# Optimization experiments

Measured on AMD Instinct MI355X. Metric: run time of the kernel, lower is better.

## Reference

```python
import jax, jax.numpy as jnp
import numpy as np

N_HEADS = 4
HEAD_DIM = 128
FMAP_H, FMAP_W = 32, 32
IN_DIM = 512
BATCH = 16


def setup_inputs() -> dict:
    key = jax.random.key(0)
    k1, k2, k3, k4 = jax.random.split(key, 4)
    scale = HEAD_DIM ** (-0.5)
    x = jax.random.normal(k1, (BATCH, IN_DIM, FMAP_H, FMAP_W), dtype=jnp.float32)
    # 1x1 conv weight producing q,k,v stacked along output channels
    conv_w = jax.random.normal(k2, (3 * N_HEADS * HEAD_DIM, IN_DIM), dtype=jnp.float32) * (IN_DIM ** -0.5)
    pos_h = jax.random.normal(k3, (FMAP_H, HEAD_DIM), dtype=jnp.float32) * scale
    pos_w = jax.random.normal(k4, (FMAP_W, HEAD_DIM), dtype=jnp.float32) * scale
    return {"x": x, "conv_w": conv_w, "pos_h": pos_h, "pos_w": pos_w}


def reference(x, conv_w, pos_h, pos_w):
    B, C, H, W = x.shape
    hw = H * W
    scale = HEAD_DIM ** (-0.5)
    # 1x1 conv == pointwise linear over channels
    qkv = jnp.einsum('bchw,oc->bohw', x, conv_w)               # [B, 3*nh*hd, H, W]
    qkv = qkv.reshape(B, 3, N_HEADS, HEAD_DIM, hw)             # chunk + per-head split
    q = jnp.swapaxes(qkv[:, 0], -1, -2) * scale                # [B, nh, hw, hd]
    k = jnp.swapaxes(qkv[:, 1], -1, -2)
    v = jnp.swapaxes(qkv[:, 2], -1, -2)
    # absolute positional embedding: h[i,:]+w[j,:] flattened over positions
    emb = (pos_h[:, None, :] + pos_w[None, :, :]).reshape(hw, HEAD_DIM)
    sim = jnp.einsum('bhid,bhjd->bhij', q, k) + jnp.einsum('bhid,jd->bhij', q, emb)
    attn = jax.nn.softmax(sim, axis=-1)
    out = jnp.einsum('bhij,bhjd->bhid', attn, v)               # [B, nh, hw, hd]
    out = jnp.swapaxes(out, -1, -2)                            # [B, nh, hd, hw]
    return out.reshape(B, N_HEADS * HEAD_DIM, hw // N_HEADS, N_HEADS)
```

## Files before the change

kernel.cpp:

```cpp
#include <hip/hip_runtime.h>

#define NB 16
#define NH 4
#define HD 128
#define HW 1024
#define CIN 512

typedef short s16x8 __attribute__((ext_vector_type(8)));
typedef short s16x4 __attribute__((ext_vector_type(4)));
typedef float f32x4 __attribute__((ext_vector_type(4)));

static __device__ __forceinline__ short f2bf(float f) {
    union { float f; unsigned u; } v; v.f = f;
    unsigned r = v.u + 0x7fffu + ((v.u >> 16) & 1u);
    return (short)(r >> 16);
}

static __device__ __forceinline__ void gload16(const short* g, short* l) {
    __builtin_amdgcn_global_load_lds(
        (const __attribute__((address_space(1))) unsigned int*)g,
        (__attribute__((address_space(3))) unsigned int*)l, 16, 0, 0);
}

__global__ __launch_bounds__(256) void prep_xw(
    const float* __restrict__ x, const float* __restrict__ w,
    short* __restrict__ xT, short* __restrict__ Wb)
{
    int blk = blockIdx.x;
    if (blk < NB * 16 * 32) {
        int b = blk >> 9, rem = blk & 511;
        int ct = rem >> 5, pt = rem & 31;
        __shared__ float tile[32][33];
        int tc = threadIdx.x >> 5;
        int tp = threadIdx.x & 31;
        const float* xb = x + ((size_t)b * CIN + ct * 32) * HW + pt * 32;
        #pragma unroll
        for (int i = 0; i < 4; i++)
            tile[tc + i * 8][tp] = xb[(size_t)(tc + i * 8) * HW + tp];
        __syncthreads();
        int p = threadIdx.x >> 3, cq = threadIdx.x & 7;
        short* xo = xT + ((size_t)b * HW + pt * 32 + p) * CIN + ct * 32 + cq * 4;
        s16x4 o4 = { f2bf(tile[cq * 4 + 0][p]), f2bf(tile[cq * 4 + 1][p]),
                     f2bf(tile[cq * 4 + 2][p]), f2bf(tile[cq * 4 + 3][p]) };
        *reinterpret_cast<s16x4*>(xo) = o4;
    } else {
        int wb = blk - NB * 16 * 32;
        size_t base = (size_t)wb * 1024 + threadIdx.x * 4;
        const float4 v = *reinterpret_cast<const float4*>(w + base);
        s16x4 o4 = { f2bf(v.x), f2bf(v.y), f2bf(v.z), f2bf(v.w) };
        *reinterpret_cast<s16x4*>(Wb + base) = o4;
    }
}

__global__ __launch_bounds__(256, 2) void qkv_proj(
    const short* __restrict__ xT, const short* __restrict__ Wb,
    const float* __restrict__ pos_h, const float* __restrict__ pos_w,
    short* __restrict__ Q, short* __restrict__ Kp, short* __restrict__ Vt)
{
    __shared__ __align__(1024) char smem[65536];
    short* As = (short*)smem;
    short* Bs = As + 2 * 128 * 64;
    short* vb = (short*)smem;
    short* T  = (short*)smem;

    const int pt = blockIdx.x, ot = blockIdx.y, b = blockIdx.z;
    const int tid = threadIdx.x;
    const int wave = tid >> 6, lane = tid & 63;
    const int l16 = lane & 15, quad = lane >> 4;
    const int wm = (wave & 1) * 64, wn = (wave >> 1) * 64;
    const int o0 = ot * 128, p0 = pt * 128;

    const short* xb = xT + (size_t)b * HW * CIN;

    const int r8 = lane >> 3, c8 = lane & 7;
    const int sch = c8 ^ r8;
    const short* wsrc = Wb + (size_t)(o0 + wave * 32 + r8) * CIN + sch * 8;
    const short* xsrc = xb + (size_t)(p0 + wave * 32 + r8) * CIN + sch * 8;

    f32x4 acc[4][4];
    #pragma unroll
    for (int i = 0; i < 4; i++)
        #pragma unroll
        for (int j = 0; j < 4; j++)
            acc[i][j] = f32x4{0.f, 0.f, 0.f, 0.f};

    #define STAGE_AB(buf, step)                                               \
        do {                                                                  \
            int kc_ = (step) * 64;                                            \
            short* ad_ = As + (buf) * 8192 + wave * 2048;                     \
            short* bd_ = Bs + (buf) * 8192 + wave * 2048;                     \
            _Pragma("unroll")                                                 \
            for (int j = 0; j < 4; j++) {                                     \
                gload16(wsrc + kc_ + (size_t)(j * 8) * CIN, ad_ + j * 512);   \
                gload16(xsrc + kc_ + (size_t)(j * 8) * CIN, bd_ + j * 512);   \
            }                                                                 \
        } while (0)

    STAGE_AB(0, 0);
    __syncthreads();

    #pragma unroll 1
    for (int st = 0; st < 8; st++) {
        const int cur = st & 1, nxt = cur ^ 1;
        const short* as = As + cur * 8192;
        const short* bs = Bs + cur * 8192;

        STAGE_AB(nxt, (st + 1) & 7);

        #pragma unroll
        for (int kk = 0; kk < 2; kk++) {
            s16x8 aF[4], bF[4];
            #pragma unroll
            for (int mi = 0; mi < 4; mi++)
                aF[mi] = *(const s16x8*)(as + (wm + mi * 16 + l16) * 64
                                         + (((kk * 4 + quad) ^ (l16 & 7)) * 8));
            #pragma unroll
            for (int ni = 0; ni < 4; ni++)
                bF[ni] = *(const s16x8*)(bs + (wn + ni * 16 + l16) * 64
                                         + (((kk * 4 + quad) ^ (l16 & 7)) * 8));
            #pragma unroll
            for (int mi = 0; mi < 4; mi++)
                #pragma unroll
                for (int ni = 0; ni < 4; ni++)
                    acc[mi][ni] = __builtin_amdgcn_mfma_f32_16x16x32_bf16(
                        aF[mi], bF[ni], acc[mi][ni], 0, 0, 0);
        }
        __syncthreads();
    }
    #undef STAGE_AB

    const int s = ot >> 2, h = ot & 3;
    const size_t bh = (size_t)(b * NH + h);

    if (s < 2) {
        const float qs = 0.08838834764831845f * 1.4426950408889634f;
        #pragma unroll
        for (int mi = 0; mi < 4; mi++) {
            int col = wm + mi * 16 + quad * 4;
            int chunk = col >> 3, sub = (quad & 1) * 4;
            #pragma unroll
            for (int ni = 0; ni < 4; ni++) {
                int row = wn + ni * 16 + l16;
                f32x4 a = acc[mi][ni];
                s16x4 o4;
                if (s == 0) {
                    o4 = s16x4{ f2bf(a.x * qs), f2bf(a.y * qs),
                                f2bf(a.z * qs), f2bf(a.w * qs) };
                } else {
                    int p = p0 + row;
                    const float4 eh = *reinterpret_cast<const float4*>(pos_h + (p >> 5) * HD + col);
                    const float4 ew = *reinterpret_cast<const float4*>(pos_w + (p & 31) * HD + col);
                    o4 = s16x4{ f2bf(a.x + eh.x + ew.x), f2bf(a.y + eh.y + ew.y),
                                f2bf(a.z + eh.z + ew.z), f2bf(a.w + eh.w + ew.w) };
                }
                *(s16x4*)(T + row * 128 + ((chunk ^ (l16 & 7)) * 8 + sub)) = o4;
            }
        }
        __syncthreads();
        short* Ob = (s == 0 ? Q : Kp) + bh * (size_t)(HW * HD) + (size_t)p0 * HD;
        #pragma unroll
        for (int j = 0; j < 8; j++) {
            int row = j * 16 + (tid >> 4);
            int c16 = tid & 15;
            s16x8 v8 = *(const s16x8*)(T + row * 128 + ((c16 ^ ((tid >> 4) & 7)) * 8));
            *reinterpret_cast<s16x8*>(Ob + (size_t)row * HD + c16 * 8) = v8;
        }
    } else {
        __syncthreads();
        #pragma unroll
        for (int mi = 0; mi < 4; mi++) {
            int d0 = wm + mi * 16 + quad * 4;
            #pragma unroll
            for (int ni = 0; ni < 4; ni++) {
                int p = wn + ni * 16 + l16;
                f32x4 a = acc[mi][ni];
                int g = p >> 5, u = p & 31;
                int slot = g * 32 + ((u & 15) >> 2) * 8 + (u >> 4) * 4 + 0;
                (void)slot;
                vb[(d0 + 0) * 136 + p] = f2bf(a.x);
                vb[(d0 + 1) * 136 + p] = f2bf(a.y);
                vb[(d0 + 2) * 136 + p] = f2bf(a.z);
                vb[(d0 + 3) * 136 + p] = f2bf(a.w);
            }
        }
        __syncthreads();
        short* Vb = Vt + bh * (size_t)(HD * HW);
        #pragma unroll
        for (int j = 0; j < 8; j++) {
            int d = j * 16 + (tid >> 4);
            int c16 = tid & 15;
            const short* row = vb + d * 136;
            int g = c16 >> 2;
            int qs = (c16 & 3) * 2 + 0;
            qs = c16 & 3;
            int base = g * 32 + qs * 4;
            s16x4 lo = *(const s16x4*)(row + base);
            s16x4 hi = *(const s16x4*)(row + base + 16);
            s16x8 v8 = { lo[0], lo[1], lo[2], lo[3],
                         hi[0], hi[1], hi[2], hi[3] };
            *reinterpret_cast<s16x8*>(Vb + (size_t)d * HW + p0 + c16 * 8) = v8;
        }
    }
}

__global__ __launch_bounds__(256, 2) void attn_fused(
    const short* __restrict__ Q, const short* __restrict__ Kp,
    const short* __restrict__ Vt, float* __restrict__ out)
{
    __shared__ __align__(1024) short Ks[2][64 * 128];
    __shared__ __align__(1024) short Vs[2][128 * 64];

    const int flat = blockIdx.x;
    const int qt = flat >> 6;
    const int bh = flat & 63;
    const int tid = threadIdx.x;
    const int wave = tid >> 6, lane = tid & 63;
    const int l16 = lane & 15, quad = lane >> 4;

    const short* Qb = Q + (size_t)bh * (HW * HD);
    const short* Kb = Kp + (size_t)bh * (HW * HD);
    const short* Vb = Vt + (size_t)bh * (HD * HW);

    const int q0 = qt * 128 + wave * 32;

    s16x8 bQ[2][4];
    #pragma unroll
    for (int nt = 0; nt < 2; nt++)
        #pragma unroll
        for (int kk = 0; kk < 4; kk++)
            bQ[nt][kk] = *(const s16x8*)(Qb + (size_t)(q0 + nt * 16 + l16) * HD
                                         + kk * 32 + quad * 8);

    s16x8 ones;
    #pragma unroll
    for (int j = 0; j < 8; j++) ones[j] = (short)0x3F80;

    f32x4 Oacc[2][8];
    #pragma unroll
    for (int mt = 0; mt < 2; mt++)
        #pragma unroll
        for (int dt = 0; dt < 8; dt++)
            Oacc[mt][dt] = f32x4{0.f, 0.f, 0.f, 0.f};
    f32x4 lacc[2] = { f32x4{0.f, 0.f, 0.f, 0.f}, f32x4{0.f, 0.f, 0.f, 0.f} };

    const int kRow = lane >> 4;
    const int vRow = lane >> 3;
    const int vSch = (lane & 7) ^ vRow;

    #define STAGE(buf, tile)                                                  \
        do {                                                                  \
            _Pragma("unroll")                                                 \
            for (int j = 0; j < 4; j++) {                                     \
                int kkey = wave * 16 + j * 4 + kRow;                          \
                gload16(Kb + ((size_t)((tile) * 64 + kkey)) * HD              \
                           + (((lane & 15) ^ (j * 4 + kRow)) * 8),            \
                        &Ks[buf][(wave * 16 + j * 4) * 128] + lane * 8);      \
                int vd = wave * 32 + j * 8 + vRow;                            \
                gload16(Vb + (size_t)vd * HW + (tile) * 64 + vSch * 8,        \
                        &Vs[buf][(wave * 32 + j * 8) * 64] + lane * 8);       \
            }                                                                 \
        } while (0)

    STAGE(0, 0);
    __syncthreads();

    #pragma unroll 1
    for (int kt = 0; kt < 16; kt++) {
        const int cur = kt & 1, nxt = cur ^ 1;
        const short* ks = Ks[cur];
        const short* vs = Vs[cur];

        STAGE(nxt, (kt + 1) & 15);

        f32x4 c[4][2];
        __builtin_amdgcn_s_setprio(1);
        #pragma unroll
        for (int mtp = 0; mtp < 4; mtp++) {
            s16x8 aK[4];
            #pragma unroll
            for (int kk = 0; kk < 4; kk++)
                aK[kk] = *(const s16x8*)(ks + (mtp * 16 + l16) * 128
                                         + (((kk * 4 + quad) ^ l16) * 8));
            c[mtp][0] = f32x4{0.f, 0.f, 0.f, 0.f};
            c[mtp][1] = f32x4{0.f, 0.f, 0.f, 0.f};
            #pragma unroll
            for (int kk = 0; kk < 4; kk++) {
                c[mtp][0] = __builtin_amdgcn_mfma_f32_16x16x32_bf16(
                    aK[kk], bQ[0][kk], c[mtp][0], 0, 0, 0);
                c[mtp][1] = __builtin_amdgcn_mfma_f32_16x16x32_bf16(
                    aK[kk], bQ[1][kk], c[mtp][1], 0, 0, 0);
            }
        }
        __builtin_amdgcn_s_setprio(0);

        #pragma unroll
        for (int h = 0; h < 2; h++) {
            s16x8 aP[2];
            #pragma unroll
            for (int mt = 0; mt < 2; mt++) {
                f32x4 e0 = c[2 * h][mt], e1 = c[2 * h + 1][mt];
                aP[mt] = s16x8{
                    f2bf(__builtin_amdgcn_exp2f(e0[0])),
                    f2bf(__builtin_amdgcn_exp2f(e0[1])),
                    f2bf(__builtin_amdgcn_exp2f(e0[2])),
                    f2bf(__builtin_amdgcn_exp2f(e0[3])),
                    f2bf(__builtin_amdgcn_exp2f(e1[0])),
                    f2bf(__builtin_amdgcn_exp2f(e1[1])),
                    f2bf(__builtin_amdgcn_exp2f(e1[2])),
                    f2bf(__builtin_amdgcn_exp2f(e1[3])) };
            }

            __builtin_amdgcn_s_setprio(1);
            #pragma unroll
            for (int mt = 0; mt < 2; mt++)
                lacc[mt] = __builtin_amdgcn_mfma_f32_16x16x32_bf16(
                    aP[mt], ones, lacc[mt], 0, 0, 0);

            #pragma unroll
            for (int dt = 0; dt < 8; dt++) {
                s16x8 bV = *(const s16x8*)(vs + (dt * 16 + l16) * 64
                                           + (((h * 4 + quad) ^ (l16 & 7)) * 8));
                #pragma unroll
                for (int mt = 0; mt < 2; mt++)
                    Oacc[mt][dt] = __builtin_amdgcn_mfma_f32_16x16x32_bf16(
                        aP[mt], bV, Oacc[mt][dt], 0, 0, 0);
            }
            __builtin_amdgcn_s_setprio(0);
        }
        __syncthreads();
    }
    #undef STAGE

    float* ob = out + (size_t)bh * (HD * HW);
    #pragma unroll
    for (int mt = 0; mt < 2; mt++) {
        float inv[4];
        #pragma unroll
        for (int r = 0; r < 4; r++) inv[r] = __builtin_amdgcn_rcpf(lacc[mt][r]);
        int prow = q0 + mt * 16 + quad * 4;
        #pragma unroll
        for (int dt = 0; dt < 8; dt++) {
            int d = dt * 16 + l16;
            f32x4 o = Oacc[mt][dt];
            float4 o4 = { o[0] * inv[0], o[1] * inv[1],
                          o[2] * inv[2], o[3] * inv[3] };
            *reinterpret_cast<float4*>(ob + (size_t)d * HW + prow) = o4;
        }
    }
}

extern "C" void kernel_launch(void* const* d_in, const int* in_sizes, int n_in,
                              void* d_out, int out_size, void* d_ws, size_t ws_size,
                              hipStream_t stream) {
    const float* x  = (const float*)d_in[0];
    const float* w  = (const float*)d_in[1];
    const float* ph = (const float*)d_in[2];
    const float* pw = (const float*)d_in[3];

    const size_t BHPD = (size_t)NB * NH * HW * HD;
    short* Q    = (short*)d_ws;
    short* Kp   = Q + BHPD;
    short* Vt   = Kp + BHPD;
    short* xT   = Vt + BHPD;
    short* Wb   = xT + (size_t)NB * HW * CIN;
    float* outp = (float*)d_out;

    prep_xw<<<dim3(NB * 16 * 32 + 768), 256, 0, stream>>>(x, w, xT, Wb);
    qkv_proj<<<dim3(8, 12, NB), 256, 0, stream>>>(xT, Wb, ph, pw, Q, Kp, Vt);
    attn_fused<<<dim3(512), 256, 0, stream>>>(Q, Kp, Vt, outp);
}
```

Measured before the change: 172.7 us.

## Single-buffer QKV projection staging to raise occupancy to four blocks per CU

Replaces the double-buffered LDS staging in the QKV projection GEMM with a single buffer, cutting shared memory from 64KB to 34KB and raising the launch-bounds occupancy hint from 2 to 4 blocks. The intent is to hide global-load latency through more resident blocks instead of in-block prefetch. In exchange, each K step now waits on its own loads before computing, and the 4-block hint may limit registers available for the 64 float accumulators per thread. Dead index code in the V epilogue is also removed.

Measured after the change: 162.4 us. -6.0%, faster.

```diff
diff --git a/kernel.cpp b/kernel.cpp
--- a/kernel.cpp
+++ b/kernel.cpp
@@ -52,14 +52,14 @@
     }
 }
 
-__global__ __launch_bounds__(256, 2) void qkv_proj(
+__global__ __launch_bounds__(256, 4) void qkv_proj(
     const short* __restrict__ xT, const short* __restrict__ Wb,
     const float* __restrict__ pos_h, const float* __restrict__ pos_w,
     short* __restrict__ Q, short* __restrict__ Kp, short* __restrict__ Vt)
 {
-    __shared__ __align__(1024) char smem[65536];
+    __shared__ __align__(1024) char smem[34816];
     short* As = (short*)smem;
-    short* Bs = As + 2 * 128 * 64;
+    short* Bs = As + 128 * 64;
     short* vb = (short*)smem;
     short* T  = (short*)smem;
 
@@ -76,6 +76,8 @@
     const int sch = c8 ^ r8;
     const short* wsrc = Wb + (size_t)(o0 + wave * 32 + r8) * CIN + sch * 8;
     const short* xsrc = xb + (size_t)(p0 + wave * 32 + r8) * CIN + sch * 8;
+    short* adst = As + wave * 2048;
+    short* bdst = Bs + wave * 2048;
 
     f32x4 acc[4][4];
     #pragma unroll
@@ -84,39 +86,24 @@
         for (int j = 0; j < 4; j++)
             acc[i][j] = f32x4{0.f, 0.f, 0.f, 0.f};
 
-    #define STAGE_AB(buf, step)                                               \
-        do {                                                                  \
-            int kc_ = (step) * 64;                                            \
-            short* ad_ = As + (buf) * 8192 + wave * 2048;                     \
-            short* bd_ = Bs + (buf) * 8192 + wave * 2048;                     \
-            _Pragma("unroll")                                                 \
-            for (int j = 0; j < 4; j++) {                                     \
-                gload16(wsrc + kc_ + (size_t)(j * 8) * CIN, ad_ + j * 512);   \
-                gload16(xsrc + kc_ + (size_t)(j * 8) * CIN, bd_ + j * 512);   \
-            }                                                                 \
-        } while (0)
-
-    STAGE_AB(0, 0);
-    __syncthreads();
-
     #pragma unroll 1
-    for (int st = 0; st < 8; st++) {
-        const int cur = st & 1, nxt = cur ^ 1;
-        const short* as = As + cur * 8192;
-        const short* bs = Bs + cur * 8192;
-
-        STAGE_AB(nxt, (st + 1) & 7);
-
+    for (int kc = 0; kc < CIN; kc += 64) {
+        #pragma unroll
+        for (int j = 0; j < 4; j++) {
+            gload16(wsrc + kc + (size_t)(j * 8) * CIN, adst + j * 512);
+            gload16(xsrc + kc + (size_t)(j * 8) * CIN, bdst + j * 512);
+        }
+        __syncthreads();
         #pragma unroll
         for (int kk = 0; kk < 2; kk++) {
             s16x8 aF[4], bF[4];
             #pragma unroll
             for (int mi = 0; mi < 4; mi++)
-                aF[mi] = *(const s16x8*)(as + (wm + mi * 16 + l16) * 64
+                aF[mi] = *(const s16x8*)(As + (wm + mi * 16 + l16) * 64
                                          + (((kk * 4 + quad) ^ (l16 & 7)) * 8));
             #pragma unroll
             for (int ni = 0; ni < 4; ni++)
-                bF[ni] = *(const s16x8*)(bs + (wn + ni * 16 + l16) * 64
+                bF[ni] = *(const s16x8*)(Bs + (wn + ni * 16 + l16) * 64
                                          + (((kk * 4 + quad) ^ (l16 & 7)) * 8));
             #pragma unroll
             for (int mi = 0; mi < 4; mi++)
@@ -127,7 +114,6 @@
         }
         __syncthreads();
     }
-    #undef STAGE_AB
 
     const int s = ot >> 2, h = ot & 3;
     const size_t bh = (size_t)(b * NH + h);
@@ -174,9 +160,6 @@
             for (int ni = 0; ni < 4; ni++) {
                 int p = wn + ni * 16 + l16;
                 f32x4 a = acc[mi][ni];
-                int g = p >> 5, u = p & 31;
-                int slot = g * 32 + ((u & 15) >> 2) * 8 + (u >> 4) * 4 + 0;
-                (void)slot;
                 vb[(d0 + 0) * 136 + p] = f2bf(a.x);
                 vb[(d0 + 1) * 136 + p] = f2bf(a.y);
                 vb[(d0 + 2) * 136 + p] = f2bf(a.z);
@@ -190,9 +173,7 @@
             int d = j * 16 + (tid >> 4);
             int c16 = tid & 15;
             const short* row = vb + d * 136;
-            int g = c16 >> 2;
-            int qs = (c16 & 3) * 2 + 0;
-            qs = c16 & 3;
+            int g = c16 >> 2, qs = c16 & 3;
             int base = g * 32 + qs * 4;
             s16x4 lo = *(const s16x4*)(row + base);
             s16x4 hi = *(const s16x4*)(row + base + 16);
```
